# Kernel optimization log

Measured on AMD Instinct MI355X. Metric: run time of the kernel, lower is better.

## Reference

```python
import jax, jax.numpy as jnp
import numpy as np

HIDDEN = 128
CHUNK = 3
EPS = 1e-5  # BatchNorm1d eps


def conv1d(x, w, b, pad):
    # x: (B, C_in, S), w: (C_out, C_in, K)
    y = jax.lax.conv_general_dilated(x, w, window_strides=(1,), padding=[(pad, pad)],
                                     dimension_numbers=('NCH', 'OIH', 'NCH'))
    return y + b[None, :, None]


def setup_inputs() -> dict:
    key = jax.random.key(0)
    ks = jax.random.split(key, 16)
    B, S = 64, 2048
    sc = 0.05
    inp = {}
    inp['x'] = jax.random.normal(ks[0], (B, S), jnp.float32)
    inp['seq_lens'] = jax.random.randint(ks[1], (B,), 0, S).astype(jnp.int64)
    # conv stack params (layer 0 has in_channels=1)
    inp['conv_w0'] = jax.random.normal(ks[2], (HIDDEN, 1, 3), jnp.float32) * sc
    inp['conv_b0'] = jax.random.normal(ks[3], (HIDDEN,), jnp.float32) * sc
    inp['conv_w1'] = jax.random.normal(ks[4], (HIDDEN, HIDDEN, 3), jnp.float32) * sc
    inp['conv_b1'] = jax.random.normal(ks[5], (HIDDEN,), jnp.float32) * sc
    inp['conv_w2'] = jax.random.normal(ks[6], (HIDDEN, HIDDEN, 3), jnp.float32) * sc
    inp['conv_b2'] = jax.random.normal(ks[7], (HIDDEN,), jnp.float32) * sc
    # BatchNorm (eval mode): gamma, beta, running mean/var, stacked over 3 layers
    inp['bn_gamma'] = 1.0 + 0.1 * jax.random.normal(ks[8], (3, HIDDEN), jnp.float32)
    inp['bn_beta'] = 0.1 * jax.random.normal(ks[9], (3, HIDDEN), jnp.float32)
    inp['bn_mean'] = 0.1 * jax.random.normal(ks[10], (3, HIDDEN), jnp.float32)
    inp['bn_var'] = jax.random.uniform(ks[11], (3, HIDDEN), jnp.float32, 0.5, 1.5)
    # pre_fc_conv: Conv1d(H, H, kernel=CHUNK) -> consumes whole chunk
    inp['pre_w'] = jax.random.normal(ks[12], (HIDDEN, HIDDEN, CHUNK), jnp.float32) * sc
    inp['pre_b'] = jax.random.normal(ks[13], (HIDDEN,), jnp.float32) * sc
    # fc: Linear(H, 1)
    inp['fc_w'] = jax.random.normal(ks[14], (1, HIDDEN), jnp.float32) * sc
    inp['fc_b'] = jax.random.normal(ks[15], (1,), jnp.float32) * sc
    return inp


def reference(x, seq_lens, conv_w0, conv_b0, conv_w1, conv_b1, conv_w2, conv_b2,
              bn_gamma, bn_beta, bn_mean, bn_var, pre_w, pre_b, fc_w, fc_b):
    h = x[:, None, :]  # (B, 1, S)
    for i, (w, b) in enumerate([(conv_w0, conv_b0), (conv_w1, conv_b1), (conv_w2, conv_b2)]):
        h = jax.nn.relu(conv1d(h, w, b, pad=1))
        # BatchNorm1d in eval mode; Dropout is identity in eval
        scale = (bn_gamma[i] / jnp.sqrt(bn_var[i] + EPS))[None, :, None]
        h = (h - bn_mean[i][None, :, None]) * scale + bn_beta[i][None, :, None]
    h = jnp.transpose(h, (0, 2, 1))  # (B, S, H)
    B, S, H = h.shape
    K = S // CHUNK  # max non-overlapping chunks per sample
    chunks = h[:, :K * CHUNK, :].reshape(B, K, CHUNK, H)  # (B, K, c, H)
    # pre_fc_conv over a length-c chunk with kernel c -> single output position
    z = jnp.einsum('bkth,oht->bko', chunks, pre_w) + pre_b  # (B, K, H)
    z = jax.nn.relu(z)
    out = jnp.einsum('bkh,oh->bko', z, fc_w) + fc_b  # (B, K, 1)
    out = out[..., 0]
    # validity mask: sample b contributes floor(seq_lens[b]/c) chunks
    n_chunks = seq_lens // CHUNK
    valid = jnp.arange(K)[None, :] < n_chunks[:, None]
    out = jnp.where(valid, out, 0.0)
    return out.reshape(-1)  # (B*K,) padded/masked version of torch's ragged concat
```

## Files before the change

### kernel.cpp

```cpp
#include <hip/hip_runtime.h>

#define BB   64
#define S    2048
#define HH   128
#define KCH  682
#define EPS  1e-5f

#define TT2   96
#define NTB2  22
#define NROWS 114

typedef __attribute__((ext_vector_type(8))) _Float16 f16x8;
typedef __attribute__((ext_vector_type(2))) __fp16 fp16v2;
typedef __attribute__((ext_vector_type(8))) unsigned short u16x8;
typedef __attribute__((ext_vector_type(4))) float f32x4;

__device__ __forceinline__ unsigned short f2h(float v) {
    union { _Float16 h; unsigned short u; } c;
    c.h = (_Float16)v;
    return c.u;
}

__device__ __forceinline__ unsigned pk2(float lo, float hi) {
    union { fp16v2 v; unsigned u; } c;
    c.v = __builtin_amdgcn_cvt_pkrtz(lo, hi);
    return c.u;
}

__global__ void pack_w_frags(const float* __restrict__ w1, const float* __restrict__ w2,
                             const float* __restrict__ pw, unsigned short* __restrict__ wpk) {
    int u = blockIdx.x * 256 + threadIdx.x;
    if (u >= 18432) return;
    int lane = u & 63, mc = (u >> 6) & 7, kb = (u >> 9) % 12, mat = u / 6144;
    const float* src = (mat == 0) ? w1 : (mat == 1) ? w2 : pw;
    int c = mc * 16 + (lane & 15);
    int kbase = kb * 32 + ((lane >> 4) << 3);
    u16x8 hv;
    #pragma unroll
    for (int j = 0; j < 8; ++j) {
        int k = kbase + j, tap = k >> 7, ci = k & 127;
        hv[j] = f2h(src[c * 384 + ci * 3 + tap]);
    }
    *(u16x8*)(wpk + (size_t)((mat * 12 + kb) * 8 + mc) * 512 + lane * 8) = hv;
}

__device__ __forceinline__ int read_seqlen(const int* seq, int b) {
    bool is64 = true;
    for (int i = 1; i < 64; i += 2) { if (seq[i] != 0) { is64 = false; break; } }
    return is64 ? seq[2 * b] : seq[b];
}

__device__ __forceinline__ int haddr(int rr, int chunk) {
    return (rr << 8) | ((chunk ^ (rr & 15)) << 4);
}

template<int NT>
__device__ __forceinline__ void conv_f16(
        f32x4 (&acc)[2][NT], const unsigned short* __restrict__ wpk, int mat,
        const unsigned short* __restrict__ hH, int cg, int nt_base, int nt_lim,
        int rbase, int lane) {
    #pragma unroll
    for (int m = 0; m < 2; ++m)
        #pragma unroll
        for (int j = 0; j < NT; ++j) acc[m][j] = (f32x4){0.f, 0.f, 0.f, 0.f};

    const f16x8* wp = (const f16x8*)wpk;
    const size_t base = (size_t)(mat * 12) * 8 + cg * 2;
    f16x8 a0 = wp[(base + 0) * 64 + lane];
    f16x8 a1 = wp[(base + 1) * 64 + lane];
    for (int kb = 0; kb < 12; ++kb) {
        f16x8 na0 = a0, na1 = a1;
        if (kb < 11) {
            const size_t nfb = base + (size_t)(kb + 1) * 8;
            na0 = wp[(nfb + 0) * 64 + lane];
            na1 = wp[(nfb + 1) * 64 + lane];
        }
        const int tap = kb >> 2;
        const int chunk = (kb & 3) * 4 + (lane >> 4);
        const int rr0 = rbase + tap + (lane & 15);
        __builtin_amdgcn_s_setprio(1);
        #pragma unroll
        for (int j = 0; j < NT; ++j) {
            const int nt = nt_base + j;
            if (nt < nt_lim) {
                const int ad = haddr(rr0 + nt * 16, chunk);
                f16x8 bh = *(const f16x8*)((const char*)hH + ad);
                acc[0][j] = __builtin_amdgcn_mfma_f32_16x16x32_f16(a0, bh, acc[0][j], 0, 0, 0);
                acc[1][j] = __builtin_amdgcn_mfma_f32_16x16x32_f16(a1, bh, acc[1][j], 0, 0, 0);
            }
        }
        __builtin_amdgcn_s_setprio(0);
        a0 = na0; a1 = na1;
    }
}

template<int NT, int ROW_OFF, int T_OFF>
__device__ __forceinline__ void epi_f16(
        f32x4 (&acc)[2][NT], const float* __restrict__ bias,
        const float* __restrict__ bng, const float* __restrict__ bnb,
        const float* __restrict__ bnm, const float* __restrict__ bnv, int layer,
        unsigned short* __restrict__ hH, int cg, int nt_base, int nt_lim,
        int lane, int t0) {
    #pragma unroll
    for (int m = 0; m < 2; ++m) {
        const int c0 = (cg * 2 + m) * 16 + (lane >> 4) * 4;
        const float4 bv = *(const float4*)&bias[c0];
        const float4 g  = *(const float4*)&bng[layer * 128 + c0];
        const float4 be = *(const float4*)&bnb[layer * 128 + c0];
        const float4 mn = *(const float4*)&bnm[layer * 128 + c0];
        const float4 vr = *(const float4*)&bnv[layer * 128 + c0];
        const float av[4] = { g.x * rsqrtf(vr.x + EPS), g.y * rsqrtf(vr.y + EPS),
                              g.z * rsqrtf(vr.z + EPS), g.w * rsqrtf(vr.w + EPS) };
        const float dv[4] = { be.x - mn.x * av[0], be.y - mn.y * av[1],
                              be.z - mn.z * av[2], be.w - mn.w * av[3] };
        const float bb[4] = { bv.x, bv.y, bv.z, bv.w };
        const int byte = c0 * 2, chunk = byte >> 4, off = byte & 15;
        #pragma unroll
        for (int j = 0; j < NT; ++j) {
            const int nt = nt_base + j;
            if (nt < nt_lim) {
                const int tt = nt * 16 + (lane & 15);
                const int t = t0 + T_OFF + tt;
                const int rr = tt + ROW_OFF;
                const bool ok = (t >= 0) && (t < S);
                float v[4];
                #pragma unroll
                for (int r = 0; r < 4; ++r) {
                    v[r] = 0.f;
                    if (ok) v[r] = fmaf(fmaxf(acc[m][j][r] + bb[r], 0.f), av[r], dv[r]);
                }
                uint2 st = { pk2(v[0], v[1]), pk2(v[2], v[3]) };
                *(uint2*)((char*)hH + (haddr(rr, chunk) | off)) = st;
            }
        }
    }
}

__global__ __launch_bounds__(512, 8)
void fused_mfma(const float* __restrict__ x, const int* __restrict__ seq,
                const float* __restrict__ w0, const float* __restrict__ b0,
                const float* __restrict__ b1, const float* __restrict__ b2,
                const float* __restrict__ bng, const float* __restrict__ bnb,
                const float* __restrict__ bnm, const float* __restrict__ bnv,
                const float* __restrict__ pb, const float* __restrict__ fcw,
                const float* __restrict__ fcb, const unsigned short* __restrict__ wpk,
                float* __restrict__ out) {
    __shared__ __align__(16) unsigned short hH[NROWS * 128];
    __shared__ __align__(16) float xs[116];
    __shared__ float p0[6 * 128];
    __shared__ float zred[4][2][16];
    __shared__ int nch_s;

    const int tid = threadIdx.x;
    const int lane = tid & 63, wv = tid >> 6;
    const int cg = wv & 3, ng = wv >> 2;
    const int b  = blockIdx.x / NTB2;
    const int jt = blockIdx.x - b * NTB2;
    const int t0 = jt * TT2;

    if (tid < 116) {
        const int t = t0 - 4 + tid;
        xs[tid] = (t >= 0 && t < S) ? x[b * S + t] : 0.f;
    }
    if (tid < 128) {
        const int c = tid;
        p0[c]         = w0[c * 3 + 0];
        p0[128 + c]   = w0[c * 3 + 1];
        p0[2*128 + c] = w0[c * 3 + 2];
        p0[3*128 + c] = b0[c];
        const float a0 = bng[c] * rsqrtf(bnv[c] + EPS);
        p0[4*128 + c] = a0;
        p0[5*128 + c] = bnb[c] - bnm[c] * a0;
    }
    if (tid == 0) nch_s = read_seqlen(seq, b) / 3;
    __syncthreads();

    for (int it = 0; it < 4; ++it) {
        const int u = tid + it * 512;
        if (u < NROWS * 16) {
            const int rr = u >> 4, oct = u & 15, ci0 = oct * 8;
            const int t = t0 - 3 + rr;
            const bool ok = (t >= 0) && (t < S);
            const float xm = xs[rr], xc = xs[rr + 1], xp = xs[rr + 2];
            float v[8];
            #pragma unroll
            for (int q = 0; q < 8; ++q) {
                const int c = ci0 + q;
                v[q] = 0.f;
                if (ok) {
                    float sa = fmaf(xp, p0[2*128 + c],
                               fmaf(xc, p0[128 + c],
                               fmaf(xm, p0[c], p0[3*128 + c])));
                    v[q] = fmaf(fmaxf(sa, 0.f), p0[4*128 + c], p0[5*128 + c]);
                }
            }
            uint4 st = { pk2(v[0], v[1]), pk2(v[2], v[3]),
                         pk2(v[4], v[5]), pk2(v[6], v[7]) };
            *(uint4*)((char*)hH + haddr(rr, oct)) = st;
        }
    }
    __syncthreads();

    {
        f32x4 acc1[2][4];
        conv_f16<4>(acc1, wpk, 0, hH, cg, ng * 4, 7, 0, lane);
        __syncthreads();
        epi_f16<4, 1, -2>(acc1, b1, bng, bnb, bnm, bnv, 1, hH, cg, ng * 4, 7, lane, t0);
    }
    __syncthreads();

    {
        f32x4 acc2[2][3];
        conv_f16<3>(acc2, wpk, 1, hH, cg, ng * 3, 6, 2, lane);
        __syncthreads();
        epi_f16<3, 3, 0>(acc2, b2, bng, bnb, bnm, bnv, 2, hH, cg, ng * 3, 6, lane, t0);
    }
    __syncthreads();

    f32x4 pacc[2];
    pacc[0] = (f32x4){0.f, 0.f, 0.f, 0.f};
    pacc[1] = (f32x4){0.f, 0.f, 0.f, 0.f};
    {
        const f16x8* wp = (const f16x8*)wpk;
        const int klocal = ng * 16 + (lane & 15);
        const size_t base = (size_t)(2 * 12) * 8 + cg * 2;
        f16x8 a0 = wp[(base + 0) * 64 + lane];
        f16x8 a1 = wp[(base + 1) * 64 + lane];
        for (int kb = 0; kb < 12; ++kb) {
            f16x8 na0 = a0, na1 = a1;
            if (kb < 11) {
                const size_t nfb = base + (size_t)(kb + 1) * 8;
                na0 = wp[(nfb + 0) * 64 + lane];
                na1 = wp[(nfb + 1) * 64 + lane];
            }
            const int tap = kb >> 2;
            const int chunk = (kb & 3) * 4 + (lane >> 4);
            const int rr = 3 + 3 * klocal + tap;
            const int ad = haddr(rr, chunk);
            f16x8 bh = *(const f16x8*)((const char*)hH + ad);
            __builtin_amdgcn_s_setprio(1);
            pacc[0] = __builtin_amdgcn_mfma_f32_16x16x32_f16(a0, bh, pacc[0], 0, 0, 0);
            pacc[1] = __builtin_amdgcn_mfma_f32_16x16x32_f16(a1, bh, pacc[1], 0, 0, 0);
            __builtin_amdgcn_s_setprio(0);
            a0 = na0; a1 = na1;
        }
    }

    float s0 = 0.f;
    #pragma unroll
    for (int m = 0; m < 2; ++m) {
        const int o0 = (cg * 2 + m) * 16 + (lane >> 4) * 4;
        const float4 pbv = *(const float4*)&pb[o0];
        const float4 fwv = *(const float4*)&fcw[o0];
        const float pbb[4] = { pbv.x, pbv.y, pbv.z, pbv.w };
        const float fww[4] = { fwv.x, fwv.y, fwv.z, fwv.w };
        #pragma unroll
        for (int r = 0; r < 4; ++r)
            s0 += fmaxf(pacc[m][r] + pbb[r], 0.f) * fww[r];
    }
    s0 += __shfl_xor(s0, 16);
    s0 += __shfl_xor(s0, 32);
    if (lane < 16) zred[cg][ng][lane] = s0;
    __syncthreads();
    if (tid < 32) {
        const int kt = tid >> 4, kl = tid & 15;
        const float zz = zred[0][kt][kl] + zred[1][kt][kl]
                       + zred[2][kt][kl] + zred[3][kt][kl];
        const int kG = jt * 32 + tid;
        if (kG < KCH)
            out[b * KCH + kG] = (kG < nch_s) ? (zz + fcb[0]) : 0.f;
    }
}

#define TT   78
#define NTB  27
#define STRIDE 84

__device__ __forceinline__ void stage_w_fb(float* __restrict__ wtS,
                                           const float* __restrict__ wraw, int cc, int tid) {
    for (int i = tid; i < 6144; i += 256)
        wtS[i] = wraw[(i & 127) * 384 + cc * 3 + (i >> 7)];
}

__device__ __forceinline__ void conv_gemm_fb(float (&acc)[10][4],
                                             const float* __restrict__ wraw,
                                             const float* __restrict__ hAp,
                                             float* __restrict__ wtS,
                                             int tid, int c0, int tbase) {
    #pragma unroll
    for (int i = 0; i < 10; ++i)
        #pragma unroll
        for (int q = 0; q < 4; ++q) acc[i][q] = 0.f;
    for (int cc = 0; cc < HH; cc += 16) {
        __syncthreads();
        stage_w_fb(wtS, wraw, cc, tid);
        __syncthreads();
        for (int ci = 0; ci < 16; ++ci) {
            float hr[12];
            #pragma unroll
            for (int j = 0; j < 12; ++j) hr[j] = hAp[(cc + ci) * STRIDE + tbase + j];
            #pragma unroll
            for (int tap = 0; tap < 3; ++tap) {
                const float4 w = *(const float4*)&wtS[((ci * 3 + tap) << 7) + c0];
                #pragma unroll
                for (int i = 0; i < 10; ++i) {
                    const float h = hr[i + tap];
                    acc[i][0] = fmaf(h, w.x, acc[i][0]);
                    acc[i][1] = fmaf(h, w.y, acc[i][1]);
                    acc[i][2] = fmaf(h, w.z, acc[i][2]);
                    acc[i][3] = fmaf(h, w.w, acc[i][3]);
                }
            }
        }
    }
}

__global__ __launch_bounds__(256, 2)
void fused_pd(const float* __restrict__ x, const int* __restrict__ seq,
              const float* __restrict__ w0, const float* __restrict__ b0,
              const float* __restrict__ w1raw, const float* __restrict__ b1,
              const float* __restrict__ w2raw, const float* __restrict__ b2,
              const float* __restrict__ bng, const float* __restrict__ bnb,
              const float* __restrict__ bnm, const float* __restrict__ bnv,
              const float* __restrict__ pwraw, const float* __restrict__ pb,
              const float* __restrict__ fcw, const float* __restrict__ fcb,
              float* __restrict__ out) {
    __shared__ __align__(16) float hA[HH * STRIDE];
    __shared__ __align__(16) float wtS[6144];
    __shared__ __align__(16) float xsf[TT + 8];
    __shared__ int nch_s;

    const int tid = threadIdx.x;
    const int b  = blockIdx.x / NTB;
    const int jt = blockIdx.x - b * NTB;
    const int t0 = jt * TT;

    for (int j = tid; j < TT + 6; j += 256) {
        const int t = t0 - 3 + j;
        xsf[j] = (t >= 0 && t < S) ? x[b * S + t] : 0.f;
    }
    if (tid == 0) nch_s = read_seqlen(seq, b) / 3;

    const int cch = tid & 127;
    const float w0a = w0[cch * 3 + 0], w0b = w0[cch * 3 + 1], w0c = w0[cch * 3 + 2];
    const float bb0 = b0[cch];
    const float a0 = bng[cch] * rsqrtf(bnv[cch] + EPS);
    const float d0 = bnb[cch] - bnm[cch] * a0;
    __syncthreads();

    for (int i = tid; i < (TT + 4) * HH; i += 256) {
        const int ttl = i >> 7;
        const int t = t0 - 2 + ttl;
        float v = 0.f;
        if (t >= 0 && t < S) {
            float sa = fmaf(xsf[ttl + 2], w0c, fmaf(xsf[ttl + 1], w0b, fmaf(xsf[ttl], w0a, bb0)));
            v = fmaf(fmaxf(sa, 0.f), a0, d0);
        }
        hA[cch * STRIDE + ttl] = v;
    }

    const int cg = tid & 31, tg = tid >> 5;
    const int c0 = cg * 4;
    const int tbase = tg * 10;
    float acc[10][4];

    conv_gemm_fb(acc, w1raw, hA, wtS, tid, c0, tbase);
    {
        const float4 bv = *(const float4*)&b1[c0];
        const float4 g  = *(const float4*)&bng[HH + c0];
        const float4 be = *(const float4*)&bnb[HH + c0];
        const float4 mn = *(const float4*)&bnm[HH + c0];
        const float4 vr = *(const float4*)&bnv[HH + c0];
        float av[4] = { g.x * rsqrtf(vr.x + EPS), g.y * rsqrtf(vr.y + EPS),
                        g.z * rsqrtf(vr.z + EPS), g.w * rsqrtf(vr.w + EPS) };
        float dv[4] = { be.x - mn.x * av[0], be.y - mn.y * av[1],
                        be.z - mn.z * av[2], be.w - mn.w * av[3] };
        float bb[4] = { bv.x, bv.y, bv.z, bv.w };
        __syncthreads();
        #pragma unroll
        for (int i = 0; i < 10; ++i) {
            const int tt2 = tbase + i;
            const int t = t0 - 1 + tt2;
            const bool ok = (t >= 0) && (t < S);
            #pragma unroll
            for (int q = 0; q < 4; ++q) {
                float v = 0.f;
                if (ok) v = fmaf(fmaxf(acc[i][q] + bb[q], 0.f), av[q], dv[q]);
                hA[(c0 + q) * STRIDE + tt2] = v;
            }
        }
        __syncthreads();
    }

    conv_gemm_fb(acc, w2raw, hA, wtS, tid, c0, tbase);
    {
        const float4 bv = *(const float4*)&b2[c0];
        const float4 g  = *(const float4*)&bng[2 * HH + c0];
        const float4 be = *(const float4*)&bnb[2 * HH + c0];
        const float4 mn = *(const float4*)&bnm[2 * HH + c0];
        const float4 vr = *(const float4*)&bnv[2 * HH + c0];
        float av[4] = { g.x * rsqrtf(vr.x + EPS), g.y * rsqrtf(vr.y + EPS),
                        g.z * rsqrtf(vr.z + EPS), g.w * rsqrtf(vr.w + EPS) };
        float dv[4] = { be.x - mn.x * av[0], be.y - mn.y * av[1],
                        be.z - mn.z * av[2], be.w - mn.w * av[3] };
        float bb[4] = { bv.x, bv.y, bv.z, bv.w };
        __syncthreads();
        #pragma unroll
        for (int i = 0; i < 10; ++i) {
            const int tt3 = tbase + i;
            if (tt3 < TT) {
                const int t = t0 + tt3;
                #pragma unroll
                for (int q = 0; q < 4; ++q) {
                    float vv = 0.f;
                    if (t < S) vv = fmaf(fmaxf(acc[i][q] + bb[q], 0.f), av[q], dv[q]);
                    hA[(c0 + q) * STRIDE + tt3] = vv;
                }
            }
        }
        __syncthreads();
    }

    const int og = tid & 31, kg = tid >> 5;
    const int oo = og * 4;
    float pacc[4][4];
    #pragma unroll
    for (int j = 0; j < 4; ++j)
        #pragma unroll
        for (int q = 0; q < 4; ++q) pacc[j][q] = 0.f;

    for (int hc = 0; hc < HH; hc += 16) {
        __syncthreads();
        stage_w_fb(wtS, pwraw, hc, tid);
        __syncthreads();
        for (int h = 0; h < 16; ++h) {
            #pragma unroll
            for (int tap = 0; tap < 3; ++tap) {
                const float4 w = *(const float4*)&wtS[((h * 3 + tap) << 7) + oo];
                #pragma unroll
                for (int j = 0; j < 4; ++j) {
                    int kl = kg * 4 + j; kl = (kl > 25) ? 25 : kl;
                    const float hv = hA[(hc + h) * STRIDE + 3 * kl + tap];
                    pacc[j][0] = fmaf(hv, w.x, pacc[j][0]);
                    pacc[j][1] = fmaf(hv, w.y, pacc[j][1]);
                    pacc[j][2] = fmaf(hv, w.z, pacc[j][2]);
                    pacc[j][3] = fmaf(hv, w.w, pacc[j][3]);
                }
            }
        }
    }

    const float fcb0 = fcb[0];
    const float4 pbv = *(const float4*)&pb[oo];
    const float4 fwv = *(const float4*)&fcw[oo];
    const int nch = nch_s;
    #pragma unroll
    for (int j = 0; j < 4; ++j) {
        float s = fmaxf(pacc[j][0] + pbv.x, 0.f) * fwv.x
                + fmaxf(pacc[j][1] + pbv.y, 0.f) * fwv.y
                + fmaxf(pacc[j][2] + pbv.z, 0.f) * fwv.z
                + fmaxf(pacc[j][3] + pbv.w, 0.f) * fwv.w;
        #pragma unroll
        for (int m = 1; m < 32; m <<= 1) s += __shfl_xor(s, m, 64);
        if (og == 0) {
            const int kl = kg * 4 + j;
            const int kG = jt * 26 + kl;
            if (kl < 26 && kG < KCH)
                out[b * KCH + kG] = (kG < nch) ? (s + fcb0) : 0.f;
        }
    }
}

extern "C" void kernel_launch(void* const* d_in, const int* in_sizes, int n_in,
                              void* d_out, int out_size, void* d_ws, size_t ws_size,
                              hipStream_t stream) {
    (void)in_sizes; (void)n_in; (void)out_size;
    const float* x    = (const float*)d_in[0];
    const int*   seq  = (const int*)d_in[1];
    const float* w0   = (const float*)d_in[2];
    const float* b0   = (const float*)d_in[3];
    const float* w1   = (const float*)d_in[4];
    const float* b1   = (const float*)d_in[5];
    const float* w2   = (const float*)d_in[6];
    const float* b2   = (const float*)d_in[7];
    const float* bng  = (const float*)d_in[8];
    const float* bnb  = (const float*)d_in[9];
    const float* bnm  = (const float*)d_in[10];
    const float* bnv  = (const float*)d_in[11];
    const float* pw   = (const float*)d_in[12];
    const float* pb   = (const float*)d_in[13];
    const float* fcw  = (const float*)d_in[14];
    const float* fcb  = (const float*)d_in[15];
    float* out = (float*)d_out;

    const size_t need = (size_t)3 * 12 * 8 * 1024;
    if (ws_size >= need) {
        unsigned short* wpk = (unsigned short*)d_ws;
        pack_w_frags<<<72, 256, 0, stream>>>(w1, w2, pw, wpk);
        fused_mfma<<<BB * NTB2, 512, 0, stream>>>(x, seq, w0, b0, b1, b2,
                                                  bng, bnb, bnm, bnv,
                                                  pb, fcw, fcb, wpk, out);
    } else {
        fused_pd<<<BB * NTB, 256, 0, stream>>>(x, seq, w0, b0, w1, b1, w2, b2,
                                               bng, bnb, bnm, bnv, pw, pb, fcw, fcb,
                                               out);
    }
}
```

Baseline: 83.97 us.

## Enlarge time tile to 120 steps and drop weight register prefetch

Each block now covers 120 time steps (40 chunks) instead of 96, giving 18 tiles per batch instead of 22 and less halo recomputation. Layer-2 conv and the pre-fc stage use 4 and up to 2 MFMA n-tiles per wave, with clamping of the partial final chunk range and a flat reduction buffer. The weight software prefetch into registers is also removed, which lowers register pressure but exposes global load latency. The larger tile raises LDS use and uneven work across wave groups in the final stage.

```diff
diff --git a/kernel.cpp b/kernel.cpp
--- a/kernel.cpp
+++ b/kernel.cpp
@@ -6,9 +6,9 @@
 #define KCH  682
 #define EPS  1e-5f
 
-#define TT2   96
-#define NTB2  22
-#define NROWS 114
+#define TT2   120
+#define NTB2  18
+#define NROWS 132
 
 typedef __attribute__((ext_vector_type(8))) _Float16 f16x8;
 typedef __attribute__((ext_vector_type(2))) __fp16 fp16v2;
@@ -65,16 +65,10 @@
         for (int j = 0; j < NT; ++j) acc[m][j] = (f32x4){0.f, 0.f, 0.f, 0.f};
 
     const f16x8* wp = (const f16x8*)wpk;
-    const size_t base = (size_t)(mat * 12) * 8 + cg * 2;
-    f16x8 a0 = wp[(base + 0) * 64 + lane];
-    f16x8 a1 = wp[(base + 1) * 64 + lane];
     for (int kb = 0; kb < 12; ++kb) {
-        f16x8 na0 = a0, na1 = a1;
-        if (kb < 11) {
-            const size_t nfb = base + (size_t)(kb + 1) * 8;
-            na0 = wp[(nfb + 0) * 64 + lane];
-            na1 = wp[(nfb + 1) * 64 + lane];
-        }
+        const size_t fb = (size_t)(mat * 12 + kb) * 8 + cg * 2;
+        f16x8 a0 = wp[(fb + 0) * 64 + lane];
+        f16x8 a1 = wp[(fb + 1) * 64 + lane];
         const int tap = kb >> 2;
         const int chunk = (kb & 3) * 4 + (lane >> 4);
         const int rr0 = rbase + tap + (lane & 15);
@@ -90,7 +84,6 @@
             }
         }
         __builtin_amdgcn_s_setprio(0);
-        a0 = na0; a1 = na1;
     }
 }
 
@@ -146,9 +139,9 @@
                 const float* __restrict__ fcb, const unsigned short* __restrict__ wpk,
                 float* __restrict__ out) {
     __shared__ __align__(16) unsigned short hH[NROWS * 128];
-    __shared__ __align__(16) float xs[116];
+    __shared__ __align__(16) float xs[136];
     __shared__ float p0[6 * 128];
-    __shared__ float zred[4][2][16];
+    __shared__ float zred[4][48];
     __shared__ int nch_s;
 
     const int tid = threadIdx.x;
@@ -157,8 +150,9 @@
     const int b  = blockIdx.x / NTB2;
     const int jt = blockIdx.x - b * NTB2;
     const int t0 = jt * TT2;
-
-    if (tid < 116) {
+    const int kb0 = jt * 40;
+
+    if (tid < 134) {
         const int t = t0 - 4 + tid;
         xs[tid] = (t >= 0 && t < S) ? x[b * S + t] : 0.f;
     }
@@ -175,7 +169,7 @@
     if (tid == 0) nch_s = read_seqlen(seq, b) / 3;
     __syncthreads();
 
-    for (int it = 0; it < 4; ++it) {
+    for (int it = 0; it < 5; ++it) {
         const int u = tid + it * 512;
         if (u < NROWS * 16) {
             const int rr = u >> 4, oct = u & 15, ci0 = oct * 8;
@@ -203,72 +197,78 @@
 
     {
         f32x4 acc1[2][4];
-        conv_f16<4>(acc1, wpk, 0, hH, cg, ng * 4, 7, 0, lane);
-        __syncthreads();
-        epi_f16<4, 1, -2>(acc1, b1, bng, bnb, bnm, bnv, 1, hH, cg, ng * 4, 7, lane, t0);
+        conv_f16<4>(acc1, wpk, 0, hH, cg, ng * 4, 8, 0, lane);
+        __syncthreads();
+        epi_f16<4, 1, -2>(acc1, b1, bng, bnb, bnm, bnv, 1, hH, cg, ng * 4, 8, lane, t0);
     }
     __syncthreads();
 
     {
-        f32x4 acc2[2][3];
-        conv_f16<3>(acc2, wpk, 1, hH, cg, ng * 3, 6, 2, lane);
-        __syncthreads();
-        epi_f16<3, 3, 0>(acc2, b2, bng, bnb, bnm, bnv, 2, hH, cg, ng * 3, 6, lane, t0);
+        f32x4 acc2[2][4];
+        conv_f16<4>(acc2, wpk, 1, hH, cg, ng * 4, 8, 2, lane);
+        __syncthreads();
+        epi_f16<4, 3, 0>(acc2, b2, bng, bnb, bnm, bnv, 2, hH, cg, ng * 4, 8, lane, t0);
     }
     __syncthreads();
 
-    f32x4 pacc[2];
-    pacc[0] = (f32x4){0.f, 0.f, 0.f, 0.f};
-    pacc[1] = (f32x4){0.f, 0.f, 0.f, 0.f};
+    const int kcount = (KCH - kb0 < 40) ? (KCH - kb0) : 40;
+    f32x4 pacc[2][2];
+    #pragma unroll
+    for (int m = 0; m < 2; ++m)
+        #pragma unroll
+        for (int j = 0; j < 2; ++j) pacc[m][j] = (f32x4){0.f, 0.f, 0.f, 0.f};
+    const int ktn = (ng == 0) ? 2 : 1;
+    const int ktb = ng * 2;
     {
         const f16x8* wp = (const f16x8*)wpk;
-        const int klocal = ng * 16 + (lane & 15);
-        const size_t base = (size_t)(2 * 12) * 8 + cg * 2;
-        f16x8 a0 = wp[(base + 0) * 64 + lane];
-        f16x8 a1 = wp[(base + 1) * 64 + lane];
         for (int kb = 0; kb < 12; ++kb) {
-            f16x8 na0 = a0, na1 = a1;
-            if (kb < 11) {
-                const size_t nfb = base + (size_t)(kb + 1) * 8;
-                na0 = wp[(nfb + 0) * 64 + lane];
-                na1 = wp[(nfb + 1) * 64 + lane];
-            }
+            const size_t fb = (size_t)(2 * 12 + kb) * 8 + cg * 2;
+            f16x8 a0 = wp[(fb + 0) * 64 + lane];
+            f16x8 a1 = wp[(fb + 1) * 64 + lane];
             const int tap = kb >> 2;
             const int chunk = (kb & 3) * 4 + (lane >> 4);
-            const int rr = 3 + 3 * klocal + tap;
-            const int ad = haddr(rr, chunk);
-            f16x8 bh = *(const f16x8*)((const char*)hH + ad);
             __builtin_amdgcn_s_setprio(1);
-            pacc[0] = __builtin_amdgcn_mfma_f32_16x16x32_f16(a0, bh, pacc[0], 0, 0, 0);
-            pacc[1] = __builtin_amdgcn_mfma_f32_16x16x32_f16(a1, bh, pacc[1], 0, 0, 0);
+            #pragma unroll
+            for (int j = 0; j < 2; ++j) {
+                if (j < ktn) {
+                    int klocal = (ktb + j) * 16 + (lane & 15);
+                    int kl = (klocal < kcount) ? klocal : (kcount - 1);
+                    const int rr = 3 * kl + tap + 3;
+                    const int ad = haddr(rr, chunk);
+                    f16x8 bh = *(const f16x8*)((const char*)hH + ad);
+                    pacc[0][j] = __builtin_amdgcn_mfma_f32_16x16x32_f16(a0, bh, pacc[0][j], 0, 0, 0);
+                    pacc[1][j] = __builtin_amdgcn_mfma_f32_16x16x32_f16(a1, bh, pacc[1][j], 0, 0, 0);
+                }
+            }
             __builtin_amdgcn_s_setprio(0);
-            a0 = na0; a1 = na1;
-        }
-    }
-
-    float s0 = 0.f;
-    #pragma unroll
-    for (int m = 0; m < 2; ++m) {
-        const int o0 = (cg * 2 + m) * 16 + (lane >> 4) * 4;
-        const float4 pbv = *(const float4*)&pb[o0];
-        const float4 fwv = *(const float4*)&fcw[o0];
-        const float pbb[4] = { pbv.x, pbv.y, pbv.z, pbv.w };
-        const float fww[4] = { fwv.x, fwv.y, fwv.z, fwv.w };
-        #pragma unroll
-        for (int r = 0; r < 4; ++r)
-            s0 += fmaxf(pacc[m][r] + pbb[r], 0.f) * fww[r];
-    }
-    s0 += __shfl_xor(s0, 16);
-    s0 += __shfl_xor(s0, 32);
-    if (lane < 16) zred[cg][ng][lane] = s0;
+        }
+    }
+
+    #pragma unroll
+    for (int j = 0; j < 2; ++j) {
+        if (j < ktn) {
+            float s0 = 0.f;
+            #pragma unroll
+            for (int m = 0; m < 2; ++m) {
+                const int o0 = (cg * 2 + m) * 16 + (lane >> 4) * 4;
+                const float4 pbv = *(const float4*)&pb[o0];
+                const float4 fwv = *(const float4*)&fcw[o0];
+                const float pbb[4] = { pbv.x, pbv.y, pbv.z, pbv.w };
+                const float fww[4] = { fwv.x, fwv.y, fwv.z, fwv.w };
+                #pragma unroll
+                for (int r = 0; r < 4; ++r)
+                    s0 += fmaxf(pacc[m][j][r] + pbb[r], 0.f) * fww[r];
+            }
+            s0 += __shfl_xor(s0, 16);
+            s0 += __shfl_xor(s0, 32);
+            if (lane < 16) zred[cg][(ktb + j) * 16 + lane] = s0;
+        }
+    }
     __syncthreads();
-    if (tid < 32) {
-        const int kt = tid >> 4, kl = tid & 15;
-        const float zz = zred[0][kt][kl] + zred[1][kt][kl]
-                       + zred[2][kt][kl] + zred[3][kt][kl];
-        const int kG = jt * 32 + tid;
-        if (kG < KCH)
-            out[b * KCH + kG] = (kG < nch_s) ? (zz + fcb[0]) : 0.f;
+    if (tid < 48 && tid < kcount) {
+        const float zz = zred[0][tid] + zred[1][tid] + zred[2][tid] + zred[3][tid];
+        const int kG = kb0 + tid;
+        out[b * KCH + kG] = (kG < nch_s) ? (zz + fcb[0]) : 0.f;
     }
 }
 
```

After: 90.75 us. +8.1%, slower.
